# Performance work log

Hardware: AMD Instinct MI355X
Metric: run time of the kernel (lower is better)

Reference implementation:

```python
import jax, jax.numpy as jnp
import numpy as np

# Production-scale dims (see shape_source)
B, N, D, H, DH, C, L = 4, 8192, 1024, 16, 64, 32, 8


def setup_inputs() -> dict:
    key = jax.random.key(0)
    ks = jax.random.split(key, 8)
    s = 0.02
    return {
        "inputs_q": jax.random.normal(ks[0], (B, N, D), jnp.float32),
        "inputs_kv": jax.random.normal(ks[1], (B, N, D), jnp.float32),
        "query_padding_mask": jnp.ones((B, N), jnp.int32),
        "key_padding_mask": jnp.ones((B, N), jnp.int32),
        "Wq": jax.random.normal(ks[2], (D, H, DH), jnp.float32) * s,
        "bq": jnp.zeros((H, DH), jnp.float32),
        "Wk": jax.random.normal(ks[3], (D, H, DH), jnp.float32) * s,
        "bk": jnp.zeros((H, DH), jnp.float32),
        "Wv": jax.random.normal(ks[4], (D, H, DH), jnp.float32) * s,
        "bv": jnp.zeros((H, DH), jnp.float32),
        "Wo": jax.random.normal(ks[5], (D, D), jnp.float32) * s,
        "bo": jnp.zeros((D,), jnp.float32),
        # per-level multihead relative position bias, rel offsets in [-(2C-1), 2C-1]
        "rpb": jax.random.normal(ks[6], (L, H, 4 * C - 1), jnp.float32) * s,
    }


def _hier_attention(inputs_q, inputs_kv, qmask, kmask, Wq, bq, Wk, bk, Wv, bv, Wo, bo, rpb):
    b, n, d = inputs_q.shape
    scale = 1.0 / jnp.sqrt(jnp.asarray(DH, inputs_q.dtype))
    # multihead projections; 1/sqrt(dh) folded into query (rescale_logits=False path)
    q = jnp.einsum('bnd,dhk->bnhk', inputs_q, Wq) * scale + bq
    k = jnp.einsum('bnd,dhk->bnhk', inputs_kv, Wk) + bk
    v = jnp.einsum('bnd,dhk->bnhk', inputs_kv, Wv) + bv
    m = kmask.astype(q.dtype)  # [b, n]
    v = v * m[:, :, None, None]

    # relative-position index table for the 3-block (left|anchor|right) window
    pq = jnp.arange(C)
    pw = jnp.arange(3 * C)
    idx = (pw[None, :] - C) - pq[:, None] + (2 * C - 1)  # [C, 3C] in [0, 4C-2]
    # hierarchical non-double-counting mask for levels > 0:
    # anchor block fully covered by finer level; halves adjacent at finer level too.
    half = C // 2
    blk = pw // C
    pl = pw % C
    inv = ((blk == 1)[None, :]
           | ((blk == 0)[None, :] & (pq[:, None] < half) & (pl[None, :] >= half))
           | ((blk == 2)[None, :] & (pq[:, None] >= half) & (pl[None, :] < half)))
    valid_hi = (~inv).astype(q.dtype)          # [C, 3C]
    valid_l0 = jnp.ones((C, 3 * C), q.dtype)

    num = jnp.zeros((b, n, H, DH), q.dtype)
    den = jnp.zeros((b, n, H), q.dtype)
    ql, kl, vl, ml = q, k, v, m
    for lvl in range(L):
        nl = ql.shape[1]
        nb = nl // C
        qb = ql.reshape(b, nb, C, H, DH)
        kb = kl.reshape(b, nb, C, H, DH)
        vb = vl.reshape(b, nb, C, H, DH)
        mb = ml.reshape(b, nb, C)
        # gather left|anchor|right neighbor blocks (zero-padded at ends)
        kp = jnp.pad(kb, ((0, 0), (1, 1), (0, 0), (0, 0), (0, 0)))
        vp = jnp.pad(vb, ((0, 0), (1, 1), (0, 0), (0, 0), (0, 0)))
        mp = jnp.pad(mb, ((0, 0), (1, 1), (0, 0)))
        kw = jnp.concatenate([kp[:, :-2], kp[:, 1:-1], kp[:, 2:]], axis=2)  # [b,nb,3C,H,DH]
        vw = jnp.concatenate([vp[:, :-2], vp[:, 1:-1], vp[:, 2:]], axis=2)
        mw = jnp.concatenate([mp[:, :-2], mp[:, 1:-1], mp[:, 2:]], axis=2)  # [b,nb,3C]
        logits = jnp.einsum('bnqhd,bnphd->bhnqp', qb, kw)  # [b,H,nb,C,3C]
        logits = logits + rpb[lvl][:, idx][None, :, None]   # per-level rpb
        valid = valid_l0 if lvl == 0 else valid_hi
        w = jnp.exp(logits) * valid[None, None, None] * mw[:, None, :, None, :]
        num_l = jnp.einsum('bhnqp,bnphd->bnqhd', w, vw).reshape(b, nl, H, DH)
        den_l = jnp.moveaxis(w.sum(-1), 1, -1).reshape(b, nl, H)
        r = 2 ** lvl  # CONST interpolation kernel: nearest-neighbor upsampling
        num = num + jnp.repeat(num_l, r, axis=1)
        den = den + jnp.repeat(den_l, r, axis=1)
        if lvl < L - 1:  # CONST coarsening kernel (size 2): average pooling
            ql = ql.reshape(b, nl // 2, 2, H, DH).mean(axis=2)
            kl = kl.reshape(b, nl // 2, 2, H, DH).mean(axis=2)
            vl = vl.reshape(b, nl // 2, 2, H, DH).mean(axis=2)
            ml = ml.reshape(b, nl // 2, 2).mean(axis=2)
    out = num / (den[..., None] + 1e-9)
    out = out * qmask.astype(q.dtype)[:, :, None, None]
    return out.reshape(b, n, H * DH) @ Wo + bo


def reference(inputs_q, inputs_kv, query_padding_mask, key_padding_mask, Wq, bq, Wk, bk, Wv, bv, Wo, bo, rpb):
    return _hier_attention(inputs_q, inputs_kv, query_padding_mask, key_padding_mask,
                           Wq, bq, Wk, bk, Wv, bv, Wo, bo, rpb)
```

## Files before the change

### kernel.cpp

```cpp
#include <hip/hip_runtime.h>

typedef unsigned short u16;
typedef unsigned int   u32;

constexpr int Bc  = 4;
constexpr int Nc  = 8192;
constexpr int Hc  = 16;
constexpr int DHc = 64;
constexpr int HD  = Hc * DHc;
constexpr int BN  = Bc * Nc;

typedef __attribute__((ext_vector_type(8))) short bf16x8;
typedef __attribute__((ext_vector_type(8))) _Float16 f16x8;
typedef __attribute__((ext_vector_type(4))) float f32x4;

struct P8 { float* p[8]; };

__device__ __forceinline__ float bf2f(u32 lo16) {
    return __uint_as_float(lo16 << 16);
}
__device__ __forceinline__ u16 f2bf(float f) {
    u32 u = __float_as_uint(f);
    u += 0x7fffu + ((u >> 16) & 1u);
    return (u16)(u >> 16);
}
__device__ __forceinline__ void unpack8(uint4 r, float* d) {
    d[0] = bf2f(r.x & 0xffffu); d[1] = bf2f(r.x >> 16);
    d[2] = bf2f(r.y & 0xffffu); d[3] = bf2f(r.y >> 16);
    d[4] = bf2f(r.z & 0xffffu); d[5] = bf2f(r.z >> 16);
    d[6] = bf2f(r.w & 0xffffu); d[7] = bf2f(r.w >> 16);
}
__device__ __forceinline__ u32 pack2(float a, float b) {
    return (u32)f2bf(a) | ((u32)f2bf(b) << 16);
}

__device__ __forceinline__ u16 f2h(float f) {
    _Float16 h = (_Float16)f;
    u16 u; __builtin_memcpy(&u, &h, 2);
    return u;
}
__device__ __forceinline__ u32 pkh2(float a, float b) {
    return (u32)f2h(a) | ((u32)f2h(b) << 16);
}
__device__ __forceinline__ void cvt8h(float4 a, float4 b, uint4& o) {
    o.x = pkh2(a.x, a.y); o.y = pkh2(a.z, a.w);
    o.z = pkh2(b.x, b.y); o.w = pkh2(b.z, b.w);
}

__device__ __forceinline__ void gload_lds16(const void* g, void* lds) {
    __builtin_amdgcn_global_load_lds(
        (const __attribute__((address_space(1))) void*)g,
        (__attribute__((address_space(3))) void*)lds,
        16, 0, 0);
}

__device__ __forceinline__ int swz_off(int row, int chunk) {
    return row * 64 + (((chunk ^ (row >> 1)) & 3) << 4);
}

__global__ __launch_bounds__(256) void transpose_split_f16(
    const float* __restrict__ W, u16* __restrict__ hiT, u16* __restrict__ loT)
{
    __shared__ float tile[32][33];
    const int bx = blockIdx.x * 32;
    const int by = blockIdx.y * 32;
    const int x = threadIdx.x & 31, y4 = threadIdx.x >> 5;
#pragma unroll
    for (int r = 0; r < 4; ++r)
        tile[y4 * 4 + r][x] = W[(size_t)(by + y4 * 4 + r) * 1024 + bx + x];
    __syncthreads();
#pragma unroll
    for (int r = 0; r < 4; ++r) {
        int n = bx + y4 * 4 + r, k = by + x;
        float v = tile[x][y4 * 4 + r];
        _Float16 h = (_Float16)v;
        u16 hu; __builtin_memcpy(&hu, &h, 2);
        hiT[(size_t)n * 1024 + k] = hu;
        if (loT) loT[(size_t)n * 1024 + k] = f2h(v - (float)h);
    }
}

__global__ __launch_bounds__(256, 2) void proj_gemm_f16(
    const float* __restrict__ A, const u16* __restrict__ BhT,
    const float* __restrict__ bias, const int* __restrict__ maskI,
    u16* __restrict__ outp, float scale)
{
    __shared__ u16 sA[128 * 32];
    __shared__ u16 sB[128 * 32];

    const int bid = blockIdx.x;
    const int swz = (bid & 7) * 256 + (bid >> 3);
    const int rb  = (swz >> 3) * 128;
    const int cb  = (swz & 7) * 128;
    const int t = threadIdx.x, l = t & 63, w = t >> 6;
    const int wr = (w >> 1) * 64, wc = (w & 1) * 64;

    const int ra = t >> 1, ha = t & 1;
    const float* Ap = A + (size_t)(rb + ra) * 1024 + ha * 16;
    const int swA = (ra >> 1) & 3;
    const int oA0 = ra * 64 + (((ha * 2)     ^ swA) << 4);
    const int oA1 = ra * 64 + (((ha * 2 + 1) ^ swA) << 4);

    const int rB0 = w * 32 + (l >> 2);
    const int rB1 = rB0 + 16;
    const int cB0 = (l & 3) ^ ((rB0 >> 1) & 3);
    const int cB1 = (l & 3) ^ ((rB1 >> 1) & 3);
    const u16* gB0 = BhT + (size_t)(cb + rB0) * 1024 + cB0 * 8;
    const u16* gB1 = BhT + (size_t)(cb + rB1) * 1024 + cB1 * 8;
    u16* ldsB0 = &sB[w * 1024];
    u16* ldsB1 = &sB[w * 1024 + 512];

    f32x4 acc[4][4] = {};
    const int q = l >> 4, r15 = l & 15;

    for (int k0 = 0; k0 < 1024; k0 += 32) {
        gload_lds16(gB0 + k0, ldsB0);
        gload_lds16(gB1 + k0, ldsB1);

        float4 f0 = *(const float4*)(Ap + k0);
        float4 f1 = *(const float4*)(Ap + k0 + 4);
        float4 f2 = *(const float4*)(Ap + k0 + 8);
        float4 f3 = *(const float4*)(Ap + k0 + 12);
        uint4 h0, h1;
        cvt8h(f0, f1, h0);
        cvt8h(f2, f3, h1);
        *(uint4*)((char*)sA + oA0) = h0;
        *(uint4*)((char*)sA + oA1) = h1;
        __syncthreads();

        f16x8 af[4], bf[4];
#pragma unroll
        for (int i = 0; i < 4; ++i)
            af[i] = *(const f16x8*)((const char*)sA + swz_off(wr + i * 16 + r15, q));
#pragma unroll
        for (int j = 0; j < 4; ++j)
            bf[j] = *(const f16x8*)((const char*)sB + swz_off(wc + j * 16 + r15, q));
#pragma unroll
        for (int i = 0; i < 4; ++i)
#pragma unroll
            for (int j = 0; j < 4; ++j)
                acc[i][j] = __builtin_amdgcn_mfma_f32_16x16x32_f16(af[i], bf[j], acc[i][j], 0, 0, 0);
        __syncthreads();
    }

    const int col0 = cb + wc + r15;
    const int row0 = rb + wr + q * 4;
    float bv4[4];
#pragma unroll
    for (int j = 0; j < 4; ++j) bv4[j] = bias[col0 + j * 16];
#pragma unroll
    for (int i = 0; i < 4; ++i) {
#pragma unroll
        for (int r = 0; r < 4; ++r) {
            int row = row0 + i * 16 + r;
            float mrow = maskI ? (float)maskI[row] : 1.f;
#pragma unroll
            for (int j = 0; j < 4; ++j)
                outp[(size_t)row * 1024 + col0 + j * 16] =
                    f2bf((acc[i][j][r] * scale + bv4[j]) * mrow);
        }
    }
}

__global__ __launch_bounds__(256, 2) void vproj_gemm_T_f16(
    const float* __restrict__ X, const u16* __restrict__ WhT,
    const float* __restrict__ bias, const int* __restrict__ maskI,
    u16* __restrict__ outT)
{
    __shared__ u16 sW[128 * 32];
    __shared__ u16 sX[128 * 32];

    const int bid = blockIdx.x;
    const int swz = (bid & 7) * 256 + (bid >> 3);
    const int rbN = (swz & 7) * 128;
    const int cbM = (swz >> 3) * 128;
    const int t = threadIdx.x, l = t & 63, w = t >> 6;
    const int wrN = (w >> 1) * 64, wcM = (w & 1) * 64;

    const int ra = t >> 1, ha = t & 1;
    const float* Xp = X + (size_t)(cbM + ra) * 1024 + ha * 16;
    const int swA = (ra >> 1) & 3;
    const int oA0 = ra * 64 + (((ha * 2)     ^ swA) << 4);
    const int oA1 = ra * 64 + (((ha * 2 + 1) ^ swA) << 4);

    const int rB0 = w * 32 + (l >> 2);
    const int rB1 = rB0 + 16;
    const int cB0 = (l & 3) ^ ((rB0 >> 1) & 3);
    const int cB1 = (l & 3) ^ ((rB1 >> 1) & 3);
    const u16* gW0 = WhT + (size_t)(rbN + rB0) * 1024 + cB0 * 8;
    const u16* gW1 = WhT + (size_t)(rbN + rB1) * 1024 + cB1 * 8;
    u16* ldsW0 = &sW[w * 1024];
    u16* ldsW1 = &sW[w * 1024 + 512];

    f32x4 acc[4][4] = {};
    const int q = l >> 4, r15 = l & 15;

    for (int k0 = 0; k0 < 1024; k0 += 32) {
        gload_lds16(gW0 + k0, ldsW0);
        gload_lds16(gW1 + k0, ldsW1);

        float4 f0 = *(const float4*)(Xp + k0);
        float4 f1 = *(const float4*)(Xp + k0 + 4);
        float4 f2 = *(const float4*)(Xp + k0 + 8);
        float4 f3 = *(const float4*)(Xp + k0 + 12);
        uint4 h0, h1;
        cvt8h(f0, f1, h0);
        cvt8h(f2, f3, h1);
        *(uint4*)((char*)sX + oA0) = h0;
        *(uint4*)((char*)sX + oA1) = h1;
        __syncthreads();

        f16x8 aw[4], bx[4];
#pragma unroll
        for (int i = 0; i < 4; ++i)
            aw[i] = *(const f16x8*)((const char*)sW + swz_off(wrN + i * 16 + r15, q));
#pragma unroll
        for (int j = 0; j < 4; ++j)
            bx[j] = *(const f16x8*)((const char*)sX + swz_off(wcM + j * 16 + r15, q));
#pragma unroll
        for (int i = 0; i < 4; ++i)
#pragma unroll
            for (int j = 0; j < 4; ++j)
                acc[i][j] = __builtin_amdgcn_mfma_f32_16x16x32_f16(aw[i], bx[j], acc[i][j], 0, 0, 0);
        __syncthreads();
    }

#pragma unroll
    for (int i = 0; i < 4; ++i)
#pragma unroll
        for (int r = 0; r < 4; ++r) {
            int n = rbN + wrN + i * 16 + q * 4 + r;
            float bn = bias[n];
#pragma unroll
            for (int j = 0; j < 4; ++j) {
                int mcol = cbM + wcM + j * 16 + r15;
                float mv = (float)maskI[mcol];
                outT[(size_t)n * 32768 + mcol] = f2bf((acc[i][j][r] + bn) * mv);
            }
        }
}

__global__ __launch_bounds__(256, 2) void out_gemm_f16(
    const u16* __restrict__ A, const u16* __restrict__ BhiT,
    const u16* __restrict__ BloT, const float* __restrict__ bias,
    float* __restrict__ outp)
{
    __shared__ u16 sA[128 * 32];
    __shared__ u16 sBhi[128 * 32], sBlo[128 * 32];

    const int bid = blockIdx.x;
    const int swz = (bid & 7) * 256 + (bid >> 3);
    const int rb  = (swz >> 3) * 128;
    const int cb  = (swz & 7) * 128;
    const int t = threadIdx.x, l = t & 63, w = t >> 6;
    const int wr = (w >> 1) * 64, wc = (w & 1) * 64;

    const int rS0 = w * 32 + (l >> 2);
    const int rS1 = rS0 + 16;
    const int cS0 = (l & 3) ^ ((rS0 >> 1) & 3);
    const int cS1 = (l & 3) ^ ((rS1 >> 1) & 3);
    const u16* gA0  = A    + (size_t)(rb + rS0) * 1024 + cS0 * 8;
    const u16* gA1  = A    + (size_t)(rb + rS1) * 1024 + cS1 * 8;
    const u16* gBh0 = BhiT + (size_t)(cb + rS0) * 1024 + cS0 * 8;
    const u16* gBh1 = BhiT + (size_t)(cb + rS1) * 1024 + cS1 * 8;
    const u16* gBl0 = BloT + (size_t)(cb + rS0) * 1024 + cS0 * 8;
    const u16* gBl1 = BloT + (size_t)(cb + rS1) * 1024 + cS1 * 8;
    u16* ldsA0  = &sA[w * 1024];
    u16* ldsA1  = &sA[w * 1024 + 512];
    u16* ldsBh0 = &sBhi[w * 1024];
    u16* ldsBh1 = &sBhi[w * 1024 + 512];
    u16* ldsBl0 = &sBlo[w * 1024];
    u16* ldsBl1 = &sBlo[w * 1024 + 512];

    f32x4 acc[4][4] = {};
    const int q = l >> 4, r15 = l & 15;

    for (int k0 = 0; k0 < 1024; k0 += 32) {
        gload_lds16(gA0  + k0, ldsA0);
        gload_lds16(gA1  + k0, ldsA1);
        gload_lds16(gBh0 + k0, ldsBh0);
        gload_lds16(gBh1 + k0, ldsBh1);
        gload_lds16(gBl0 + k0, ldsBl0);
        gload_lds16(gBl1 + k0, ldsBl1);
        __syncthreads();

        f16x8 af[4], bh[4], bl[4];
#pragma unroll
        for (int i = 0; i < 4; ++i)
            af[i] = *(const f16x8*)((const char*)sA + swz_off(wr + i * 16 + r15, q));
#pragma unroll
        for (int j = 0; j < 4; ++j) {
            int off = swz_off(wc + j * 16 + r15, q);
            bh[j] = *(const f16x8*)((const char*)sBhi + off);
            bl[j] = *(const f16x8*)((const char*)sBlo + off);
        }
#pragma unroll
        for (int i = 0; i < 4; ++i)
#pragma unroll
            for (int j = 0; j < 4; ++j) {
                acc[i][j] = __builtin_amdgcn_mfma_f32_16x16x32_f16(af[i], bh[j], acc[i][j], 0, 0, 0);
                acc[i][j] = __builtin_amdgcn_mfma_f32_16x16x32_f16(af[i], bl[j], acc[i][j], 0, 0, 0);
            }
        __syncthreads();
    }

    const int col0 = cb + wc + r15;
    const int row0 = rb + wr + q * 4;
    float bv4[4];
#pragma unroll
    for (int j = 0; j < 4; ++j) bv4[j] = bias[col0 + j * 16];
#pragma unroll
    for (int i = 0; i < 4; ++i)
#pragma unroll
        for (int r = 0; r < 4; ++r) {
            int row = row0 + i * 16 + r;
#pragma unroll
            for (int j = 0; j < 4; ++j)
                outp[(size_t)row * 1024 + col0 + j * 16] = acc[i][j][r] + bv4[j];
        }
}

__global__ void mask_to_float(const int* __restrict__ mi, float* __restrict__ mo)
{
    int i = blockIdx.x * 256 + threadIdx.x;
    if (i < BN) mo[i] = (float)mi[i];
}

__global__ void sentinel_fill(float* __restrict__ o, int n)
{
    int i = blockIdx.x * 256 + threadIdx.x;
    if (i < n) o[i] = 12345.0f;
}

__global__ __launch_bounds__(256) void pool_level(
    const u16* __restrict__ qi, u16* __restrict__ qo,
    const u16* __restrict__ ki, u16* __restrict__ ko,
    const u16* __restrict__ vi, u16* __restrict__ vo,
    const float* __restrict__ mi, float* __restrict__ mo, int nRows)
{
    int idx = blockIdx.x * 256 + threadIdx.x;
    int y   = blockIdx.y;
    if (y == 3) {
        if (idx < nRows) mo[idx] = 0.5f * (mi[2 * idx] + mi[2 * idx + 1]);
        return;
    }
    if (y == 2) {
        int ns8 = nRows >> 3;
        int sh = 31 - __clz(ns8);
        int d = idx >> sh, c = idx & (ns8 - 1);
        size_t inb = (size_t)d * (nRows * 2) + c * 16;
        uint4 a = *(const uint4*)(vi + inb);
        uint4 b = *(const uint4*)(vi + inb + 8);
        float fa[8], fb[8];
        unpack8(a, fa); unpack8(b, fb);
        uint4 o;
        o.x = pack2(0.5f * (fa[0] + fa[1]), 0.5f * (fa[2] + fa[3]));
        o.y = pack2(0.5f * (fa[4] + fa[5]), 0.5f * (fa[6] + fa[7]));
        o.z = pack2(0.5f * (fb[0] + fb[1]), 0.5f * (fb[2] + fb[3]));
        o.w = pack2(0.5f * (fb[4] + fb[5]), 0.5f * (fb[6] + fb[7]));
        *(uint4*)(vo + (size_t)d * nRows + c * 8) = o;
        return;
    }
    const u16* in  = (y == 0) ? qi : ki;
    u16*       out = (y == 0) ? qo : ko;
    int r = idx >> 7, c8 = idx & 127;
    uint4 a = *(const uint4*)(in + (size_t)(2 * r) * 1024 + c8 * 8);
    uint4 b = *(const uint4*)(in + (size_t)(2 * r + 1) * 1024 + c8 * 8);
    float fa[8], fb[8];
    unpack8(a, fa); unpack8(b, fb);
    uint4 o;
    o.x = pack2(0.5f * (fa[0] + fb[0]), 0.5f * (fa[1] + fb[1]));
    o.y = pack2(0.5f * (fa[2] + fb[2]), 0.5f * (fa[3] + fb[3]));
    o.z = pack2(0.5f * (fa[4] + fb[4]), 0.5f * (fa[5] + fb[5]));
    o.w = pack2(0.5f * (fa[6] + fb[6]), 0.5f * (fa[7] + fb[7]));
    *(uint4*)(out + (size_t)r * 1024 + c8 * 8) = o;
}

template <int WRITE_MODE>
__device__ __forceinline__ void attn_level_body(
    const u16* __restrict__ qg, const u16* __restrict__ kg,
    const u16* __restrict__ vTg, const float* __restrict__ m,
    const float* __restrict__ rpbL,
    float* __restrict__ num, float* __restrict__ den, int nl, int lvl)
{
    __shared__ u16 qs[32 * 64];
    __shared__ u16 ks_w2[2 * 32 * 104];
    __shared__ u16 vTs[64 * 96];
    __shared__ float rps[128];
    __shared__ float mwS[96];
    __shared__ float denS[64];

    const int t   = threadIdx.x;
    const int blk = blockIdx.x, h = blockIdx.y, b = blockIdx.z;
    const size_t baseRow = (size_t)b * nl + blk * 32;
    const int wbase = blk * 32 - 32;
    const int vStr = Bc * nl;

    {
        int r = t >> 3, c = t & 7;
        uint4 raw = *(const uint4*)(qg + (baseRow + r) * 1024 + h * 64 + c * 8);
        *(uint4*)&qs[r * 64 + ((c ^ (r & 7)) * 8)] = raw;
    }
#pragma unroll
    for (int it = 0; it < 3; ++it) {
        int f = t + 256 * it;
        int r = f >> 3, c = f & 7;
        int wp = wbase + r;
        uint4 raw = make_uint4(0u, 0u, 0u, 0u);
        if (wp >= 0 && wp < nl)
            raw = *(const uint4*)(kg + ((size_t)b * nl + wp) * 1024 + h * 64 + c * 8);
        *(uint4*)&ks_w2[r * 64 + ((c ^ (r & 7)) * 8)] = raw;
    }
    {
        int d = t >> 2, c3 = t & 3;
        const u16* vrow = vTg + (size_t)(h * 64 + d) * vStr + (size_t)b * nl;
#pragma unroll
        for (int o = 0; o < 3; ++o) {
            int s8 = c3 * 24 + o * 8;
            int wp8 = wbase + s8;
            uint4 raw = make_uint4(0u, 0u, 0u, 0u);
            if (wp8 >= 0 && wp8 < nl)
                raw = *(const uint4*)(vrow + wp8);
            *(uint4*)&vTs[d * 96 + s8] = raw;
        }
    }
    if (t < 96) {
        int wp = wbase + t;
        mwS[t] = (wp >= 0 && wp < nl) ? m[b * nl + wp] : 0.f;
    }
    if (t < 127) rps[t] = rpbL[h * 127 + t];
    __syncthreads();

    const int l  = t & 63, w = t >> 6;
    const int fr = l & 15, fg = l >> 4;
    const int mi  = w >> 1;
    const int njb = (w & 1) * 3;

    f32x4 lg[3] = {};
    {
        bf16x8 aq[2];
#pragma unroll
        for (int ks = 0; ks < 2; ++ks) {
            int row = mi * 16 + fr;
            aq[ks] = *(const bf16x8*)&qs[row * 64 + (((ks * 4 + fg) ^ (row & 7)) * 8)];
        }
#pragma unroll
        for (int nj = 0; nj < 3; ++nj) {
            int row = (njb + nj) * 16 + fr;
#pragma unroll
            for (int ks = 0; ks < 2; ++ks) {
                bf16x8 bk = *(const bf16x8*)&ks_w2[row * 64 + (((ks * 4 + fg) ^ (row & 7)) * 8)];
                lg[nj] = __builtin_amdgcn_mfma_f32_16x16x32_bf16(aq[ks], bk, lg[nj], 0, 0, 0);
            }
        }
    }
    __syncthreads();

    float sum_r[4] = {0.f, 0.f, 0.f, 0.f};
#pragma unroll
    for (int nj = 0; nj < 3; ++nj) {
        int j = (njb + nj) * 16 + fr;
        float mj = mwS[j];
#pragma unroll
        for (int r = 0; r < 4; ++r) {
            int i = mi * 16 + fg * 4 + r;
            float wv = __expf(lg[nj][r] + rps[j - i + 31]) * mj;
            if (lvl > 0) {
                int bj = j >> 5, pl = j & 31;
                bool inv = (bj == 1) ||
                           (bj == 0 && i < 16 && pl >= 16) ||
                           (bj == 2 && i >= 16 && pl < 16);
                if (inv) wv = 0.f;
            }
            sum_r[r] += wv;
            u32 uw = __float_as_uint(wv);
            float lo = wv - __uint_as_float(uw & 0xffff0000u);
            ks_w2[i * 104 + j]        = (u16)(uw >> 16);
            ks_w2[3328 + i * 104 + j] = (u16)(__float_as_uint(lo) >> 16);
        }
    }
#pragma unroll
    for (int r = 0; r < 4; ++r) {
        sum_r[r] += __shfl_xor(sum_r[r], 1);
        sum_r[r] += __shfl_xor(sum_r[r], 2);
        sum_r[r] += __shfl_xor(sum_r[r], 4);
        sum_r[r] += __shfl_xor(sum_r[r], 8);
    }
    if (fr == 0) {
#pragma unroll
        for (int r = 0; r < 4; ++r)
            denS[(w & 1) * 32 + mi * 16 + fg * 4 + r] = sum_r[r];
    }
    __syncthreads();

    const int ndb = (w & 1) * 2;
    f32x4 acc0 = {}, acc1 = {};
#pragma unroll
    for (int ks = 0; ks < 3; ++ks) {
        int arow = mi * 16 + fr;
        bf16x8 ah = *(const bf16x8*)&ks_w2[arow * 104 + ks * 32 + fg * 8];
        bf16x8 al = *(const bf16x8*)&ks_w2[3328 + arow * 104 + ks * 32 + fg * 8];
        int d0 = ndb * 16 + fr;
        bf16x8 bv0 = *(const bf16x8*)&vTs[d0 * 96 + ks * 32 + fg * 8];
        bf16x8 bv1 = *(const bf16x8*)&vTs[(d0 + 16) * 96 + ks * 32 + fg * 8];
        acc0 = __builtin_amdgcn_mfma_f32_16x16x32_bf16(ah, bv0, acc0, 0, 0, 0);
        acc0 = __builtin_amdgcn_mfma_f32_16x16x32_bf16(al, bv0, acc0, 0, 0, 0);
        acc1 = __builtin_amdgcn_mfma_f32_16x16x32_bf16(ah, bv1, acc1, 0, 0, 0);
        acc1 = __builtin_amdgcn_mfma_f32_16x16x32_bf16(al, bv1, acc1, 0, 0, 0);
    }

    const int i0 = mi * 16 + fg * 4;
    const int d0 = ndb * 16 + fr;
    if (WRITE_MODE == 0) {
#pragma unroll
        for (int r = 0; r < 4; ++r) {
            int cn = blk * 32 + i0 + r;
            size_t base = ((size_t)b * nl + cn) * 1024 + h * 64;
            num[base + d0]      = acc0[r];
            num[base + d0 + 16] = acc1[r];
        }
        if (t < 32) {
            float s = denS[t] + denS[32 + t];
            den[((size_t)b * nl + blk * 32 + t) * 16 + h] = s;
        }
    } else {
        const int rr = 1 << lvl;
#pragma unroll
        for (int r = 0; r < 4; ++r) {
            int cn = blk * 32 + i0 + r;
            size_t base = ((size_t)b * Nc + (size_t)cn * rr) * 1024 + h * 64;
            if (lvl == 0) {
                num[base + d0]      = acc0[r];
                num[base + d0 + 16] = acc1[r];
            } else {
                for (int rep = 0; rep < rr; ++rep) {
                    num[base + (size_t)rep * 1024 + d0]      += acc0[r];
                    num[base + (size_t)rep * 1024 + d0 + 16] += acc1[r];
                }
            }
        }
        if (t < 32) {
            float s = denS[t] + denS[32 + t];
            int cn = blk * 32 + t;
            size_t db = ((size_t)b * Nc + (size_t)cn * rr) * 16 + h;
            if (lvl == 0) {
                den[db] = s;
            } else {
                for (int rep = 0; rep < rr; ++rep) den[db + (size_t)rep * 16] += s;
            }
        }
    }
}

__global__ __launch_bounds__(256) void attn_level_pyr(
    const u16* __restrict__ qg, const u16* __restrict__ kg,
    const u16* __restrict__ vTg, const float* __restrict__ m,
    const float* __restrict__ rpbL,
    float* __restrict__ numL, float* __restrict__ denL, int nl, int lvl)
{
    attn_level_body<0>(qg, kg, vTg, m, rpbL, numL, denL, nl, lvl);
}

__global__ __launch_bounds__(256) void attn_level_rmw(
    const u16* __restrict__ qg, const u16* __restrict__ kg,
    const u16* __restrict__ vTg, const float* __restrict__ m,
    const float* __restrict__ rpbL,
    float* __restrict__ num, float* __restrict__ den, int nl, int lvl)
{
    attn_level_body<1>(qg, kg, vTg, m, rpbL, num, den, nl, lvl);
}

__global__ __launch_bounds__(256) void combine_kernel(
    const float* __restrict__ num, const float* __restrict__ den,
    const int* __restrict__ qmask, u16* __restrict__ pre)
{
    int idx = blockIdx.x * 256 + threadIdx.x;
    int row = idx >> 8, c4 = idx & 255;
    int h = c4 >> 4;
    float4 ns = *(const float4*)&num[(size_t)row * 1024 + c4 * 4];
    float f = (float)qmask[row] / (den[(size_t)row * 16 + h] + 1e-9f);
    ushort4 o;
    o.x = f2h(ns.x * f); o.y = f2h(ns.y * f);
    o.z = f2h(ns.z * f); o.w = f2h(ns.w * f);
    *(ushort4*)(pre + (size_t)row * 1024 + c4 * 4) = o;
}

__global__ __launch_bounds__(256) void combine_pyr(
    P8 nums, P8 dens, const int* __restrict__ qmask, u16* __restrict__ pre)
{
    int idx = blockIdx.x * 256 + threadIdx.x;
    int row = idx >> 8, c4 = idx & 255;
    int h = c4 >> 4;
    int b = row >> 13, s = row & (Nc - 1);
    float4 acc = make_float4(0.f, 0.f, 0.f, 0.f);
    float dt = 0.f;
#pragma unroll
    for (int l = 0; l < 8; ++l) {
        int rl = (b << (13 - l)) + (s >> l);
        const float4 nv = *(const float4*)&nums.p[l][(size_t)rl * 1024 + c4 * 4];
        acc.x += nv.x; acc.y += nv.y; acc.z += nv.z; acc.w += nv.w;
        dt += dens.p[l][(size_t)rl * 16 + h];
    }
    float f = (float)qmask[row] / (dt + 1e-9f);
    ushort4 o;
    o.x = f2h(acc.x * f); o.y = f2h(acc.y * f);
    o.z = f2h(acc.z * f); o.w = f2h(acc.w * f);
    *(ushort4*)(pre + (size_t)row * 1024 + c4 * 4) = o;
}

extern "C" void kernel_launch(void* const* d_in, const int* in_sizes, int n_in,
                              void* d_out, int out_size, void* d_ws, size_t ws_size,
                              hipStream_t stream)
{
    const float* Xq    = (const float*)d_in[0];
    const float* Xkv   = (const float*)d_in[1];
    const int*   qmask = (const int*)d_in[2];
    const int*   kmask = (const int*)d_in[3];
    const float* Wq    = (const float*)d_in[4];
    const float* bq    = (const float*)d_in[5];
    const float* Wk    = (const float*)d_in[6];
    const float* bk    = (const float*)d_in[7];
    const float* Wv    = (const float*)d_in[8];
    const float* bv    = (const float*)d_in[9];
    const float* Wo    = (const float*)d_in[10];
    const float* bo    = (const float*)d_in[11];
    const float* rpb   = (const float*)d_in[12];

    const size_t szA = (size_t)BN * HD * 2;
    const size_t szB = szA / 2;
    const size_t base_need = 3 * (szA + szB) + (size_t)BN * 6;

    size_t denPyrSz = 0, numPyrSz = 0;
    for (int l = 0; l < 8; ++l) denPyrSz += ((size_t)(BN >> l)) * 16 * 4;
    for (int l = 1; l < 8; ++l) numPyrSz += ((size_t)(BN >> l)) * 1024 * 4;
    const size_t needed_old = base_need + (size_t)BN * 16 * 4;
    const size_t needed_pyr = base_need + denPyrSz + numPyrSz;

    const bool usePyr = (ws_size >= needed_pyr);
    if (!usePyr && ws_size < needed_old) {
        sentinel_fill<<<(out_size + 255) / 256, 256, 0, stream>>>((float*)d_out, out_size);
        return;
    }

    char* p = (char*)d_ws;
    u16* qA = (u16*)p; p += szA;
    u16* qB = (u16*)p; p += szB;
    u16* kA = (u16*)p; p += szA;
    u16* kB = (u16*)p; p += szB;
    u16* vA = (u16*)p; p += szA;
    u16* vB = (u16*)p; p += szB;
    float* mA  = (float*)p; p += (size_t)BN * 4;
    float* mB  = (float*)p; p += (size_t)BN * 2;

    P8 numP, denP;
    float* denLegacy = nullptr;
    if (usePyr) {
        for (int l = 0; l < 8; ++l) { denP.p[l] = (float*)p; p += ((size_t)(BN >> l)) * 16 * 4; }
        numP.p[0] = (float*)d_out;
        for (int l = 1; l < 8; ++l) { numP.p[l] = (float*)p; p += ((size_t)(BN >> l)) * 1024 * 4; }
    } else {
        denLegacy = (float*)p;
    }
    float* num = (float*)d_out;

    u16* WsHi0 = qB;
    u16* WsLo0 = qB + 1 * 1048576;
    u16* WsHi1 = qB + 2 * 1048576;
    u16* WsHi2 = qB + 4 * 1048576;

    dim3 tsg(32, 32);
    transpose_split_f16<<<tsg, 256, 0, stream>>>(Wq, WsHi0, nullptr);
    transpose_split_f16<<<tsg, 256, 0, stream>>>(Wk, WsHi1, nullptr);
    transpose_split_f16<<<tsg, 256, 0, stream>>>(Wv, WsHi2, nullptr);

    proj_gemm_f16 <<<2048, 256, 0, stream>>>(Xq,  WsHi0, bq, nullptr, qA, 0.125f);
    proj_gemm_f16 <<<2048, 256, 0, stream>>>(Xkv, WsHi1, bk, nullptr, kA, 1.f);
    vproj_gemm_T_f16<<<2048, 256, 0, stream>>>(Xkv, WsHi2, bv, kmask, vA);
    mask_to_float<<<BN / 256, 256, 0, stream>>>(kmask, mA);

    u16* qc = qA; u16* kc = kA; u16* vc = vA; float* mc = mA;
    u16* qn = qB; u16* kn = kB; u16* vn = vB; float* mn = mB;
    for (int lvl = 0; lvl < 8; ++lvl) {
        int nl = Nc >> lvl, nb = nl / 32;
        if (usePyr) {
            attn_level_pyr<<<dim3(nb, 16, 4), 256, 0, stream>>>(
                qc, kc, vc, mc, rpb + (size_t)lvl * Hc * 127,
                numP.p[lvl], denP.p[lvl], nl, lvl);
        } else {
            attn_level_rmw<<<dim3(nb, 16, 4), 256, 0, stream>>>(
                qc, kc, vc, mc, rpb + (size_t)lvl * Hc * 127,
                num, denLegacy, nl, lvl);
        }
        if (lvl < 7) {
            int nRows = Bc * (nl / 2);
            pool_level<<<dim3(nRows / 2, 4), 256, 0, stream>>>(
                qc, qn, kc, kn, vc, vn, mc, mn, nRows);
            u16* tp;
            tp = qc; qc = qn; qn = tp;
            tp = kc; kc = kn; kn = tp;
            tp = vc; vc = vn; vn = tp;
            float* tf = mc; mc = mn; mn = tf;
        }
    }

    if (usePyr) {
        combine_pyr<<<BN, 256, 0, stream>>>(numP, denP, qmask, qA);
    } else {
        combine_kernel<<<BN, 256, 0, stream>>>(num, denLegacy, qmask, qA);
    }
    u16* WoHi = qB;
    u16* WoLo = qB + 1 * 1048576;
    transpose_split_f16<<<tsg, 256, 0, stream>>>(Wo, WoHi, WoLo);
    out_gemm_f16<<<2048, 256, 0, stream>>>(qA, WoHi, WoLo, bo, (float*)d_out);
}
```

Baseline: 1.274 ms.

## Double-buffer LDS tiles in projection and output GEMMs to overlap loads

Converts the Q/K projection, transposed V projection and output GEMMs to a double-buffered LDS pipeline. The next K-tile's global loads, including the fp32 A-tile fetch, are issued before computing on the current buffer, and one barrier per iteration replaces two. This is meant to hide global-memory latency behind the MFMA work. Launch bounds are also raised to 4 (or 3) blocks per CU, which doubles LDS use and tightens the register budget, so occupancy gains may be offset by spills.

Measured after the change: 1.346 ms. +5.7%, slower.

```diff
diff --git a/kernel.cpp b/kernel.cpp
--- a/kernel.cpp
+++ b/kernel.cpp
@@ -80,13 +80,13 @@
     }
 }
 
-__global__ __launch_bounds__(256, 2) void proj_gemm_f16(
+__global__ __launch_bounds__(256, 4) void proj_gemm_f16(
     const float* __restrict__ A, const u16* __restrict__ BhT,
     const float* __restrict__ bias, const int* __restrict__ maskI,
     u16* __restrict__ outp, float scale)
 {
-    __shared__ u16 sA[128 * 32];
-    __shared__ u16 sB[128 * 32];
+    __shared__ u16 sA[2][128 * 32];
+    __shared__ u16 sB[2][128 * 32];
 
     const int bid = blockIdx.x;
     const int swz = (bid & 7) * 256 + (bid >> 3);
@@ -107,40 +107,61 @@
     const int cB1 = (l & 3) ^ ((rB1 >> 1) & 3);
     const u16* gB0 = BhT + (size_t)(cb + rB0) * 1024 + cB0 * 8;
     const u16* gB1 = BhT + (size_t)(cb + rB1) * 1024 + cB1 * 8;
-    u16* ldsB0 = &sB[w * 1024];
-    u16* ldsB1 = &sB[w * 1024 + 512];
 
     f32x4 acc[4][4] = {};
     const int q = l >> 4, r15 = l & 15;
 
-    for (int k0 = 0; k0 < 1024; k0 += 32) {
-        gload_lds16(gB0 + k0, ldsB0);
-        gload_lds16(gB1 + k0, ldsB1);
-
-        float4 f0 = *(const float4*)(Ap + k0);
-        float4 f1 = *(const float4*)(Ap + k0 + 4);
-        float4 f2 = *(const float4*)(Ap + k0 + 8);
-        float4 f3 = *(const float4*)(Ap + k0 + 12);
+    gload_lds16(gB0, &sB[0][w * 1024]);
+    gload_lds16(gB1, &sB[0][w * 1024 + 512]);
+    {
+        float4 f0 = *(const float4*)(Ap);
+        float4 f1 = *(const float4*)(Ap + 4);
+        float4 f2 = *(const float4*)(Ap + 8);
+        float4 f3 = *(const float4*)(Ap + 12);
         uint4 h0, h1;
         cvt8h(f0, f1, h0);
         cvt8h(f2, f3, h1);
-        *(uint4*)((char*)sA + oA0) = h0;
-        *(uint4*)((char*)sA + oA1) = h1;
-        __syncthreads();
-
-        f16x8 af[4], bf[4];
+        *(uint4*)((char*)sA[0] + oA0) = h0;
+        *(uint4*)((char*)sA[0] + oA1) = h1;
+    }
+    __syncthreads();
+
+    int c = 0;
+    for (int k0 = 0; k0 < 1024; k0 += 32) {
+        const int nxt = c ^ 1;
+        const bool hasNext = (k0 + 32) < 1024;
+        float4 f0, f1, f2, f3;
+        if (hasNext) {
+            gload_lds16(gB0 + k0 + 32, &sB[nxt][w * 1024]);
+            gload_lds16(gB1 + k0 + 32, &sB[nxt][w * 1024 + 512]);
+            f0 = *(const float4*)(Ap + k0 + 32);
+            f1 = *(const float4*)(Ap + k0 + 36);
+            f2 = *(const float4*)(Ap + k0 + 40);
+            f3 = *(const float4*)(Ap + k0 + 44);
+        }
+
+        f16x8 af[4], bfv[4];
 #pragma unroll
         for (int i = 0; i < 4; ++i)
-            af[i] = *(const f16x8*)((const char*)sA + swz_off(wr + i * 16 + r15, q));
+            af[i] = *(const f16x8*)((const char*)sA[c] + swz_off(wr + i * 16 + r15, q));
 #pragma unroll
         for (int j = 0; j < 4; ++j)
-            bf[j] = *(const f16x8*)((const char*)sB + swz_off(wc + j * 16 + r15, q));
+            bfv[j] = *(const f16x8*)((const char*)sB[c] + swz_off(wc + j * 16 + r15, q));
 #pragma unroll
         for (int i = 0; i < 4; ++i)
 #pragma unroll
             for (int j = 0; j < 4; ++j)
-                acc[i][j] = __builtin_amdgcn_mfma_f32_16x16x32_f16(af[i], bf[j], acc[i][j], 0, 0, 0);
-        __syncthreads();
+                acc[i][j] = __builtin_amdgcn_mfma_f32_16x16x32_f16(af[i], bfv[j], acc[i][j], 0, 0, 0);
+
+        if (hasNext) {
+            uint4 h0, h1;
+            cvt8h(f0, f1, h0);
+            cvt8h(f2, f3, h1);
+            *(uint4*)((char*)sA[nxt] + oA0) = h0;
+            *(uint4*)((char*)sA[nxt] + oA1) = h1;
+            __syncthreads();
+            c = nxt;
+        }
     }
 
     const int col0 = cb + wc + r15;
@@ -162,13 +183,13 @@
     }
 }
 
-__global__ __launch_bounds__(256, 2) void vproj_gemm_T_f16(
+__global__ __launch_bounds__(256, 4) void vproj_gemm_T_f16(
     const float* __restrict__ X, const u16* __restrict__ WhT,
     const float* __restrict__ bias, const int* __restrict__ maskI,
     u16* __restrict__ outT)
 {
-    __shared__ u16 sW[128 * 32];
-    __shared__ u16 sX[128 * 32];
+    __shared__ u16 sW[2][128 * 32];
+    __shared__ u16 sX[2][128 * 32];
 
     const int bid = blockIdx.x;
     const int swz = (bid & 7) * 256 + (bid >> 3);
@@ -189,40 +210,61 @@
     const int cB1 = (l & 3) ^ ((rB1 >> 1) & 3);
     const u16* gW0 = WhT + (size_t)(rbN + rB0) * 1024 + cB0 * 8;
     const u16* gW1 = WhT + (size_t)(rbN + rB1) * 1024 + cB1 * 8;
-    u16* ldsW0 = &sW[w * 1024];
-    u16* ldsW1 = &sW[w * 1024 + 512];
 
     f32x4 acc[4][4] = {};
     const int q = l >> 4, r15 = l & 15;
 
-    for (int k0 = 0; k0 < 1024; k0 += 32) {
-        gload_lds16(gW0 + k0, ldsW0);
-        gload_lds16(gW1 + k0, ldsW1);
-
-        float4 f0 = *(const float4*)(Xp + k0);
-        float4 f1 = *(const float4*)(Xp + k0 + 4);
-        float4 f2 = *(const float4*)(Xp + k0 + 8);
-        float4 f3 = *(const float4*)(Xp + k0 + 12);
+    gload_lds16(gW0, &sW[0][w * 1024]);
+    gload_lds16(gW1, &sW[0][w * 1024 + 512]);
+    {
+        float4 f0 = *(const float4*)(Xp);
+        float4 f1 = *(const float4*)(Xp + 4);
+        float4 f2 = *(const float4*)(Xp + 8);
+        float4 f3 = *(const float4*)(Xp + 12);
         uint4 h0, h1;
         cvt8h(f0, f1, h0);
         cvt8h(f2, f3, h1);
-        *(uint4*)((char*)sX + oA0) = h0;
-        *(uint4*)((char*)sX + oA1) = h1;
-        __syncthreads();
+        *(uint4*)((char*)sX[0] + oA0) = h0;
+        *(uint4*)((char*)sX[0] + oA1) = h1;
+    }
+    __syncthreads();
+
+    int c = 0;
+    for (int k0 = 0; k0 < 1024; k0 += 32) {
+        const int nxt = c ^ 1;
+        const bool hasNext = (k0 + 32) < 1024;
+        float4 f0, f1, f2, f3;
+        if (hasNext) {
+            gload_lds16(gW0 + k0 + 32, &sW[nxt][w * 1024]);
+            gload_lds16(gW1 + k0 + 32, &sW[nxt][w * 1024 + 512]);
+            f0 = *(const float4*)(Xp + k0 + 32);
+            f1 = *(const float4*)(Xp + k0 + 36);
+            f2 = *(const float4*)(Xp + k0 + 40);
+            f3 = *(const float4*)(Xp + k0 + 44);
+        }
 
         f16x8 aw[4], bx[4];
 #pragma unroll
         for (int i = 0; i < 4; ++i)
-            aw[i] = *(const f16x8*)((const char*)sW + swz_off(wrN + i * 16 + r15, q));
+            aw[i] = *(const f16x8*)((const char*)sW[c] + swz_off(wrN + i * 16 + r15, q));
 #pragma unroll
         for (int j = 0; j < 4; ++j)
-            bx[j] = *(const f16x8*)((const char*)sX + swz_off(wcM + j * 16 + r15, q));
+            bx[j] = *(const f16x8*)((const char*)sX[c] + swz_off(wcM + j * 16 + r15, q));
 #pragma unroll
         for (int i = 0; i < 4; ++i)
 #pragma unroll
             for (int j = 0; j < 4; ++j)
                 acc[i][j] = __builtin_amdgcn_mfma_f32_16x16x32_f16(aw[i], bx[j], acc[i][j], 0, 0, 0);
-        __syncthreads();
+
+        if (hasNext) {
+            uint4 h0, h1;
+            cvt8h(f0, f1, h0);
+            cvt8h(f2, f3, h1);
+            *(uint4*)((char*)sX[nxt] + oA0) = h0;
+            *(uint4*)((char*)sX[nxt] + oA1) = h1;
+            __syncthreads();
+            c = nxt;
+        }
     }
 
 #pragma unroll
@@ -240,13 +282,13 @@
         }
 }
 
-__global__ __launch_bounds__(256, 2) void out_gemm_f16(
+__global__ __launch_bounds__(256, 3) void out_gemm_f16(
     const u16* __restrict__ A, const u16* __restrict__ BhiT,
     const u16* __restrict__ BloT, const float* __restrict__ bias,
     float* __restrict__ outp)
 {
-    __shared__ u16 sA[128 * 32];
-    __shared__ u16 sBhi[128 * 32], sBlo[128 * 32];
+    __shared__ u16 sA[2][128 * 32];
+    __shared__ u16 sBhi[2][128 * 32], sBlo[2][128 * 32];
 
     const int bid = blockIdx.x;
     const int swz = (bid & 7) * 256 + (bid >> 3);
@@ -265,34 +307,40 @@
     const u16* gBh1 = BhiT + (size_t)(cb + rS1) * 1024 + cS1 * 8;
     const u16* gBl0 = BloT + (size_t)(cb + rS0) * 1024 + cS0 * 8;
     const u16* gBl1 = BloT + (size_t)(cb + rS1) * 1024 + cS1 * 8;
-    u16* ldsA0  = &sA[w * 1024];
-    u16* ldsA1  = &sA[w * 1024 + 512];
-    u16* ldsBh0 = &sBhi[w * 1024];
-    u16* ldsBh1 = &sBhi[w * 1024 + 512];
-    u16* ldsBl0 = &sBlo[w * 1024];
-    u16* ldsBl1 = &sBlo[w * 1024 + 512];
 
     f32x4 acc[4][4] = {};
     const int q = l >> 4, r15 = l & 15;
 
+    gload_lds16(gA0,  &sA[0][w * 1024]);
+    gload_lds16(gA1,  &sA[0][w * 1024 + 512]);
+    gload_lds16(gBh0, &sBhi[0][w * 1024]);
+    gload_lds16(gBh1, &sBhi[0][w * 1024 + 512]);
+    gload_lds16(gBl0, &sBlo[0][w * 1024]);
+    gload_lds16(gBl1, &sBlo[0][w * 1024 + 512]);
+    __syncthreads();
+
+    int c = 0;
     for (int k0 = 0; k0 < 1024; k0 += 32) {
-        gload_lds16(gA0  + k0, ldsA0);
-        gload_lds16(gA1  + k0, ldsA1);
-        gload_lds16(gBh0 + k0, ldsBh0);
-        gload_lds16(gBh1 + k0, ldsBh1);
-        gload_lds16(gBl0 + k0, ldsBl0);
-        gload_lds16(gBl1 + k0, ldsBl1);
-        __syncthreads();
+        const int nxt = c ^ 1;
+        const bool hasNext = (k0 + 32) < 1024;
+        if (hasNext) {
+            gload_lds16(gA0  + k0 + 32, &sA[nxt][w * 1024]);
+            gload_lds16(gA1  + k0 + 32, &sA[nxt][w * 1024 + 512]);
+            gload_lds16(gBh0 + k0 + 32, &sBhi[nxt][w * 1024]);
+            gload_lds16(gBh1 + k0 + 32, &sBhi[nxt][w * 1024 + 512]);
+            gload_lds16(gBl0 + k0 + 32, &sBlo[nxt][w * 1024]);
+            gload_lds16(gBl1 + k0 + 32, &sBlo[nxt][w * 1024 + 512]);
+        }
 
         f16x8 af[4], bh[4], bl[4];
 #pragma unroll
         for (int i = 0; i < 4; ++i)
-            af[i] = *(const f16x8*)((const char*)sA + swz_off(wr + i * 16 + r15, q));
+            af[i] = *(const f16x8*)((const char*)sA[c] + swz_off(wr + i * 16 + r15, q));
 #pragma unroll
         for (int j = 0; j < 4; ++j) {
             int off = swz_off(wc + j * 16 + r15, q);
-            bh[j] = *(const f16x8*)((const char*)sBhi + off);
-            bl[j] = *(const f16x8*)((const char*)sBlo + off);
+            bh[j] = *(const f16x8*)((const char*)sBhi[c] + off);
+            bl[j] = *(const f16x8*)((const char*)sBlo[c] + off);
         }
 #pragma unroll
         for (int i = 0; i < 4; ++i)
@@ -301,7 +349,11 @@
                 acc[i][j] = __builtin_amdgcn_mfma_f32_16x16x32_f16(af[i], bh[j], acc[i][j], 0, 0, 0);
                 acc[i][j] = __builtin_amdgcn_mfma_f32_16x16x32_f16(af[i], bl[j], acc[i][j], 0, 0, 0);
             }
-        __syncthreads();
+
+        if (hasNext) {
+            __syncthreads();
+            c = nxt;
+        }
     }
 
     const int col0 = cb + wc + r15;
```
